# Kernel tuning notes

Measured on AMD Instinct MI355X. Metric: run time of the kernel, lower is better.

The kernel has to match this reference:

```python
import jax, jax.numpy as jnp
import numpy as np

N_NODES = 50000
N_EDGES = 800000
HIDDEN = 128
IN_DIM = 128
OUT_DIM = 1
N_LAYERS = 4
N_GRAPHS = 32
LN_EPS = 1e-5


def setup_inputs() -> dict:
    key = jax.random.key(0)
    ks = jax.random.split(key, 12)
    s = 1.0 / np.sqrt(HIDDEN)
    inp = {
        "x": jax.random.normal(ks[0], (N_NODES, IN_DIM), dtype=jnp.float32),
        "edge_index": jax.random.randint(ks[1], (2, N_EDGES), 0, N_NODES, dtype=jnp.int64),
        "batch": jnp.sort(jax.random.randint(ks[2], (N_NODES,), 0, N_GRAPHS, dtype=jnp.int64)),
        "W_emb": jax.random.normal(ks[3], (HIDDEN, IN_DIM), dtype=jnp.float32) * s,
        "b_emb": jax.random.normal(ks[4], (HIDDEN,), dtype=jnp.float32) * s,
        "W_layers": jax.random.normal(ks[5], (N_LAYERS, HIDDEN, HIDDEN), dtype=jnp.float32) * s,
        "b_layers": jax.random.normal(ks[6], (N_LAYERS, HIDDEN), dtype=jnp.float32) * s,
        "ln_gamma": 1.0 + 0.02 * jax.random.normal(ks[7], (N_LAYERS, HIDDEN), dtype=jnp.float32),
        "ln_beta": 0.02 * jax.random.normal(ks[8], (N_LAYERS, HIDDEN), dtype=jnp.float32),
        "W_out": jax.random.normal(ks[9], (OUT_DIM, HIDDEN), dtype=jnp.float32) * s,
    }
    return inp


def _layer_norm(x, gamma, beta):
    mu = jnp.mean(x, axis=-1, keepdims=True)
    var = jnp.mean(jnp.square(x - mu), axis=-1, keepdims=True)
    return (x - mu) * jax.lax.rsqrt(var + LN_EPS) * gamma + beta


def reference(x, edge_index, batch, W_emb, b_emb, W_layers, b_layers, ln_gamma, ln_beta, W_out):
    n = x.shape[0]
    # add self-loops (PyG GCNConv default)
    loop = jnp.arange(n, dtype=edge_index.dtype)
    row = jnp.concatenate([edge_index[0], loop])  # source nodes
    col = jnp.concatenate([edge_index[1], loop])  # target nodes
    # symmetric normalization: deg over targets
    deg = jax.ops.segment_sum(jnp.ones_like(col, dtype=x.dtype), col, num_segments=n)
    dis = jnp.where(deg > 0, jax.lax.rsqrt(jnp.maximum(deg, 1.0)), 0.0)
    norm = dis[row] * dis[col]  # [E+N]

    h = x @ W_emb.T + b_emb  # embedding layer
    for i in range(N_LAYERS):
        t = h @ W_layers[i].T                      # [N, H] linear first
        msg = t[row] * norm[:, None]               # gather + scale  [E+N, H]
        agg = jax.ops.segment_sum(msg, col, num_segments=n) + b_layers[i]
        h = _layer_norm(h + jax.nn.relu(agg), ln_gamma[i], ln_beta[i])

    out = h @ W_out.T                              # [N, OUT_DIM]
    sums = jax.ops.segment_sum(out, batch, num_segments=N_GRAPHS)
    cnts = jax.ops.segment_sum(jnp.ones((n,), out.dtype), batch, num_segments=N_GRAPHS)
    return sums / jnp.maximum(cnts, 1.0)[:, None]  # [N_GRAPHS, OUT_DIM]
```

## Files before the change

### kernel.cpp

```cpp
#include <hip/hip_runtime.h>
#include <hip/hip_fp16.h>

#define NN 50000
#define NE 800000
#define NETOT (NE + NN)
#define NH 128
#define NG 32
#define NL 4
#define NB 196
#define EMBB 782
#define HISTB 3125
#define PREP4B 256
#define LBLK 782
#define NTILE 12500
#define WSLOT (NH * NH)

typedef __attribute__((ext_vector_type(8))) short bf16x8;
typedef __attribute__((ext_vector_type(4))) float f32x4;
typedef __attribute__((ext_vector_type(2))) float f32x2;

__device__ inline short f2bf(float x) {
  union { float f; unsigned u; } v;
  v.f = x;
  unsigned r = v.u + 0x7FFF + ((v.u >> 16) & 1);
  return (short)(r >> 16);
}
__device__ inline float bf2f(short s) {
  union { unsigned u; float f; } v;
  v.u = ((unsigned)(unsigned short)s) << 16;
  return v.f;
}

__device__ inline int pdw(int t, int quad) {
  return (((2 * t + (quad >> 1)) & 3) << 3) + ((t >> 1) << 1) + (quad & 1);
}

__device__ inline void fp8row_fma(float (&ag)[4][8], uint4 qa, uint4 qb,
                                  float w) {
  const unsigned dw[8] = {qa.x, qa.y, qa.z, qa.w, qb.x, qb.y, qb.z, qb.w};
#pragma unroll
  for (int ks = 0; ks < 4; ++ks) {
    f32x2 u0 = __builtin_amdgcn_cvt_pk_f32_fp8(dw[2 * ks], 0);
    f32x2 u1 = __builtin_amdgcn_cvt_pk_f32_fp8(dw[2 * ks], 1);
    f32x2 u2 = __builtin_amdgcn_cvt_pk_f32_fp8(dw[2 * ks + 1], 0);
    f32x2 u3 = __builtin_amdgcn_cvt_pk_f32_fp8(dw[2 * ks + 1], 1);
    ag[ks][0] += u0.x * w; ag[ks][1] += u0.y * w;
    ag[ks][2] += u1.x * w; ag[ks][3] += u1.y * w;
    ag[ks][4] += u2.x * w; ag[ks][5] += u2.y * w;
    ag[ks][6] += u3.x * w; ag[ks][7] += u3.y * w;
  }
}

__device__ inline int block_exscan(int v) {
  __shared__ int wsum[4];
  int tid = threadIdx.x, wave = tid >> 6, lane = tid & 63;
  int x = v;
#pragma unroll
  for (int off = 1; off < 64; off <<= 1) {
    int y = __shfl_up(x, off, 64);
    if (lane >= off) x += y;
  }
  if (lane == 63) wsum[wave] = x;
  __syncthreads();
  int wp = 0;
  if (wave > 0) wp += wsum[0];
  if (wave > 1) wp += wsum[1];
  if (wave > 2) wp += wsum[2];
  return wp + x - v;
}

__global__ __launch_bounds__(256) void prep_hist_emb_kernel(
    const float* __restrict__ Xf, const float* __restrict__ W_emb,
    const float* __restrict__ W_layers, short* __restrict__ hi,
    short* __restrict__ lo, const int* __restrict__ row,
    const int* __restrict__ col, int* __restrict__ cnt4, int* __restrict__ rank,
    const float* __restrict__ bias, __half* __restrict__ hnew,
    unsigned char* __restrict__ h8) {
  __shared__ short Wh[WSLOT];
  __shared__ short Wl[WSLOT];
  int tid = threadIdx.x;
  int blk = blockIdx.x;
  if (blk >= EMBB) {
    if (blk < EMBB + HISTB) {
      int e = (blk - EMBB) * 256 + tid;
      if (e < NE) {
        int s = row[e];
        int t = s / NTILE;
        rank[e] = atomicAdd(&cnt4[col[e] * 4 + t], 1);
      }
    } else {
      int i = (blk - EMBB - HISTB) * 256 + tid;
      if (i < 4 * WSLOT) {
        int slot = i >> 14, f = i & (WSLOT - 1);
        int j = f & 7, lane = (f >> 3) & 63, tt = (f >> 9) & 7, ks = f >> 12;
        int n = tt * 16 + (lane & 15);
        int k = ks * 32 + ((lane >> 4) & 3) * 8 + j;
        const float* W = W_layers + (size_t)slot * WSLOT;
        float x = W[n * NH + k];
        short hh = f2bf(x);
        hi[i] = hh;
        lo[i] = f2bf(x - bf2f(hh));
      }
    }
    return;
  }

#pragma unroll
  for (int i = tid * 8; i < WSLOT; i += 256 * 8) {
    int f = i;
    int lane8 = (f >> 3) & 63, tt = (f >> 9) & 7, ks = f >> 12;
    int n = tt * 16 + (lane8 & 15);
    int k0 = ks * 32 + ((lane8 >> 4) & 3) * 8;
    const float* wr = W_emb + n * NH + k0;
    float4 a0 = *(const float4*)wr;
    float4 a1 = *(const float4*)(wr + 4);
    float wv[8] = {a0.x, a0.y, a0.z, a0.w, a1.x, a1.y, a1.z, a1.w};
    bf16x8 vh, vl;
#pragma unroll
    for (int j = 0; j < 8; ++j) {
      short hh = f2bf(wv[j]);
      vh[j] = hh;
      vl[j] = f2bf(wv[j] - bf2f(hh));
    }
    *(bf16x8*)&Wh[i] = vh;
    *(bf16x8*)&Wl[i] = vl;
  }
  __syncthreads();

  int wave = tid >> 6, lane = tid & 63;
  int quad = lane >> 4, r16 = lane & 15;
  int m0 = blk * 64 + wave * 16;
  if (m0 >= NN) return;
  int mA = m0 + r16;

  f32x4 acc[8];
#pragma unroll
  for (int t = 0; t < 8; ++t) acc[t] = (f32x4){0.f, 0.f, 0.f, 0.f};

#pragma unroll
  for (int ks = 0; ks < 4; ++ks) {
    int klane = ks * 32 + quad * 8;
    const float* xr = Xf + (size_t)mA * NH + klane;
    float4 a0 = *(const float4*)xr;
    float4 a1 = *(const float4*)(xr + 4);
    float af[8] = {a0.x, a0.y, a0.z, a0.w, a1.x, a1.y, a1.z, a1.w};
    bf16x8 xhi, xlo;
#pragma unroll
    for (int j = 0; j < 8; ++j) {
      short h = f2bf(af[j]);
      xhi[j] = h;
      xlo[j] = f2bf(af[j] - bf2f(h));
    }
#pragma unroll
    for (int t = 0; t < 8; ++t) {
      int fidx = ((ks * 8 + t) * 64 + lane) << 3;
      bf16x8 whi = *(const bf16x8*)&Wh[fidx];
      bf16x8 wlo = *(const bf16x8*)&Wl[fidx];
      acc[t] = __builtin_amdgcn_mfma_f32_16x16x32_bf16(whi, xhi, acc[t], 0, 0, 0);
      acc[t] = __builtin_amdgcn_mfma_f32_16x16x32_bf16(whi, xlo, acc[t], 0, 0, 0);
      acc[t] = __builtin_amdgcn_mfma_f32_16x16x32_bf16(wlo, xhi, acc[t], 0, 0, 0);
    }
  }

  int m = m0 + r16;
  int cb = quad * 4;
#pragma unroll
  for (int t = 0; t < 8; ++t) {
    int ch = t * 16 + cb;
    float4 bb = *(const float4*)(bias + ch);
    float o0 = acc[t][0] + bb.x, o1 = acc[t][1] + bb.y;
    float o2 = acc[t][2] + bb.z, o3 = acc[t][3] + bb.w;
    __half2 p01 = __float22half2_rn(make_float2(o0, o1));
    __half2 p23 = __float22half2_rn(make_float2(o2, o3));
    *(uint2*)(hnew + (size_t)m * NH + ch) =
        make_uint2(*(unsigned*)&p01, *(unsigned*)&p23);
    int v = 0;
    v = __builtin_amdgcn_cvt_pk_fp8_f32(o0, o1, v, 0);
    v = __builtin_amdgcn_cvt_pk_fp8_f32(o2, o3, v, 1);
    ((unsigned*)(h8 + (size_t)m * NH))[pdw(t, quad)] = (unsigned)v;
  }
}

__global__ __launch_bounds__(256) void scan1_kernel(const int* __restrict__ cnt4,
                                                    int* __restrict__ bsum,
                                                    float* __restrict__ dis,
                                                    int* __restrict__ deg) {
  int i = blockIdx.x * 256 + threadIdx.x;
  int v = 0;
  if (i < NN) {
    int4 c4 = *(const int4*)&cnt4[i * 4];
    v = c4.x + c4.y + c4.z + c4.w + 1;
    deg[i] = v;
    dis[i] = rsqrtf((float)v);
  }
  int lane = threadIdx.x & 63;
  int s = v;
#pragma unroll
  for (int off = 32; off; off >>= 1) s += __shfl_down(s, off, 64);
  __shared__ int ws[4];
  if (lane == 0) ws[threadIdx.x >> 6] = s;
  __syncthreads();
  if (threadIdx.x == 0) bsum[blockIdx.x] = ws[0] + ws[1] + ws[2] + ws[3];
}

__global__ __launch_bounds__(256) void scan3b_kernel(const int* __restrict__ deg,
                                                     const int* __restrict__ bsum,
                                                     const float* __restrict__ dis,
                                                     int* __restrict__ offs,
                                                     int2* __restrict__ csr) {
  __shared__ int ws2[4];
  int tid = threadIdx.x;
  int b = blockIdx.x;
  int v = (tid < NB && tid < b) ? bsum[tid] : 0;
  int lane = tid & 63;
  int s = v;
#pragma unroll
  for (int off = 32; off; off >>= 1) s += __shfl_down(s, off, 64);
  if (lane == 0) ws2[tid >> 6] = s;
  __syncthreads();
  int bo = ws2[0] + ws2[1] + ws2[2] + ws2[3];
  int i = b * 256 + tid;
  int c = (i < NN) ? deg[i] : 0;
  int ex = block_exscan(c);
  if (i < NN) {
    int o = bo + ex;
    offs[i] = o;
    float dii = dis[i];
    csr[o + c - 1] =
        make_int2((i << 6) | (i & 63), __float_as_int(dii * dii));
  }
}

__global__ __launch_bounds__(256) void fill_kernel(const int* __restrict__ row,
                                                   const int* __restrict__ col,
                                                   const int* __restrict__ rank,
                                                   const int* __restrict__ cnt4,
                                                   const float* __restrict__ dis,
                                                   const int* __restrict__ offs,
                                                   int2* __restrict__ csr) {
  int e = blockIdx.x * 256 + threadIdx.x;
  if (e < NE) {
    int d = col[e];
    int s = row[e];
    int t = s / NTILE;
    int4 c4 = *(const int4*)&cnt4[d * 4];
    int pre = (t > 0 ? c4.x : 0) + (t > 1 ? c4.y : 0) + (t > 2 ? c4.z : 0);
    int pos = offs[d] + pre + rank[e];
    csr[pos] =
        make_int2((s << 6) | (d & 63), __float_as_int(dis[s] * dis[d]));
  }
}

template <bool LAST>
__global__ __launch_bounds__(256) void layer_fused(
    const unsigned char* __restrict__ h8in, const short* __restrict__ Whi,
    const short* __restrict__ Wlo, const float* __restrict__ bias,
    const __half* __restrict__ hprev, const float* __restrict__ gamma,
    const float* __restrict__ beta, const float* __restrict__ Wout,
    const int* __restrict__ offs, const int2* __restrict__ csr,
    __half* __restrict__ hnew, unsigned char* __restrict__ h8out,
    float* __restrict__ nodeval) {
  int tid = threadIdx.x, wave = tid >> 6, lane = tid & 63;
  int quad = lane >> 4, r16 = lane & 15;
  int m0 = blockIdx.x * 64 + wave * 16;
  if (m0 >= NN) return;
  int nd = m0 + r16;

  float ag[4][8];
#pragma unroll
  for (int ks = 0; ks < 4; ++ks)
#pragma unroll
    for (int j = 0; j < 8; ++j) ag[ks][j] = 0.f;

  const char* rbase = (const char*)h8in + quad * 32;
  int s0 = offs[nd];
  int e1 = (nd + 1 < NN) ? offs[nd + 1] : NETOT;
  int j = s0;
  for (; j + 2 <= e1; j += 2) {
    int2 p0 = csr[j], p1 = csr[j + 1];
    const uint4* r0 = (const uint4*)(rbase + (size_t)(((unsigned)p0.x) >> 6) * NH);
    const uint4* r1 = (const uint4*)(rbase + (size_t)(((unsigned)p1.x) >> 6) * NH);
    uint4 a0 = r0[0], b0 = r0[1];
    uint4 a1 = r1[0], b1 = r1[1];
    fp8row_fma(ag, a0, b0, __int_as_float(p0.y));
    fp8row_fma(ag, a1, b1, __int_as_float(p1.y));
  }
  if (j < e1) {
    int2 p0 = csr[j];
    const uint4* r0 = (const uint4*)(rbase + (size_t)(((unsigned)p0.x) >> 6) * NH);
    uint4 a0 = r0[0], b0 = r0[1];
    fp8row_fma(ag, a0, b0, __int_as_float(p0.y));
  }

  f32x4 acc[8];
#pragma unroll
  for (int t = 0; t < 8; ++t) acc[t] = (f32x4){0.f, 0.f, 0.f, 0.f};

#pragma unroll
  for (int ks = 0; ks < 4; ++ks) {
    bf16x8 xhi, xlo;
#pragma unroll
    for (int q = 0; q < 8; ++q) {
      short hh = f2bf(ag[ks][q]);
      xhi[q] = hh;
      xlo[q] = f2bf(ag[ks][q] - bf2f(hh));
    }
#pragma unroll
    for (int t = 0; t < 8; ++t) {
      int fidx = ((ks * 8 + t) * 64 + lane) << 3;
      bf16x8 whi = *(const bf16x8*)&Whi[fidx];
      bf16x8 wlo = *(const bf16x8*)&Wlo[fidx];
      acc[t] = __builtin_amdgcn_mfma_f32_16x16x32_bf16(whi, xhi, acc[t], 0, 0, 0);
      acc[t] = __builtin_amdgcn_mfma_f32_16x16x32_bf16(whi, xlo, acc[t], 0, 0, 0);
      acc[t] = __builtin_amdgcn_mfma_f32_16x16x32_bf16(wlo, xhi, acc[t], 0, 0, 0);
    }
  }

  int m = nd;
  int cb = quad * 4;
  float vv[8][4];
  float s = 0.f, s2 = 0.f;
#pragma unroll
  for (int t = 0; t < 8; ++t) {
    int ch = t * 16 + cb;
    float4 bb = *(const float4*)(bias + ch);
    uint2 hp = *(const uint2*)(hprev + (size_t)m * NH + ch);
    float2 h01 = __half22float2(*(__half2*)&hp.x);
    float2 h23 = __half22float2(*(__half2*)&hp.y);
    float hv[4] = {h01.x, h01.y, h23.x, h23.y};
    float bb4[4] = {bb.x, bb.y, bb.z, bb.w};
#pragma unroll
    for (int r = 0; r < 4; ++r) {
      float z = fmaxf(acc[t][r] + bb4[r], 0.f);
      float val = hv[r] + z;
      vv[t][r] = val;
      s += val;
      s2 += val * val;
    }
  }
  s += __shfl_xor(s, 16, 64);
  s += __shfl_xor(s, 32, 64);
  s2 += __shfl_xor(s2, 16, 64);
  s2 += __shfl_xor(s2, 32, 64);
  float mean = s * (1.f / 128.f);
  float var = fmaxf(s2 * (1.f / 128.f) - mean * mean, 0.f);
  float inv = rsqrtf(var + 1e-5f);
  float d = 0.f;
#pragma unroll
  for (int t = 0; t < 8; ++t) {
    int ch = t * 16 + cb;
    float4 gv = *(const float4*)(gamma + ch);
    float4 bt = *(const float4*)(beta + ch);
    float o0 = (vv[t][0] - mean) * inv * gv.x + bt.x;
    float o1 = (vv[t][1] - mean) * inv * gv.y + bt.y;
    float o2 = (vv[t][2] - mean) * inv * gv.z + bt.z;
    float o3 = (vv[t][3] - mean) * inv * gv.w + bt.w;
    if (!LAST) {
      __half2 p01 = __float22half2_rn(make_float2(o0, o1));
      __half2 p23 = __float22half2_rn(make_float2(o2, o3));
      *(uint2*)(hnew + (size_t)m * NH + ch) =
          make_uint2(*(unsigned*)&p01, *(unsigned*)&p23);
      int pv = 0;
      pv = __builtin_amdgcn_cvt_pk_fp8_f32(o0, o1, pv, 0);
      pv = __builtin_amdgcn_cvt_pk_fp8_f32(o2, o3, pv, 1);
      ((unsigned*)(h8out + (size_t)m * NH))[pdw(t, quad)] = (unsigned)pv;
    } else {
      float4 wv = *(const float4*)(Wout + ch);
      d += o0 * wv.x + o1 * wv.y + o2 * wv.z + o3 * wv.w;
    }
  }
  if (LAST) {
    d += __shfl_xor(d, 16, 64);
    d += __shfl_xor(d, 32, 64);
    if (lane < 16) nodeval[m] = d;
  }
}

__global__ __launch_bounds__(256) void reduce_pool_kernel(
    const float* __restrict__ nodeval, const int* __restrict__ batch,
    float* __restrict__ gsum, int* __restrict__ gcnt, int* __restrict__ done,
    float* __restrict__ out) {
  __shared__ float bins[NG];
  __shared__ int cbins[NG];
  __shared__ int lastflag;
  int tid = threadIdx.x;
  if (tid < NG) {
    bins[tid] = 0.f;
    cbins[tid] = 0;
  }
  __syncthreads();
  int i = blockIdx.x * 256 + tid;
  if (i < NN) {
    int g = batch[i];
    atomicAdd(&bins[g], nodeval[i]);
    atomicAdd(&cbins[g], 1);
  }
  __syncthreads();
  if (tid < NG && cbins[tid]) {
    atomicAdd(&gsum[tid], bins[tid]);
    atomicAdd(&gcnt[tid], cbins[tid]);
  }
  __threadfence();
  if (tid == 0) lastflag = (atomicAdd(done, 1) == (int)gridDim.x - 1);
  __syncthreads();
  if (lastflag && tid < NG) {
    float sv = atomicAdd(&gsum[tid], 0.f);
    int cv = atomicAdd(&gcnt[tid], 0);
    out[tid] = sv / fmaxf((float)cv, 1.0f);
  }
}

extern "C" void kernel_launch(void* const* d_in, const int* in_sizes, int n_in,
                              void* d_out, int out_size, void* d_ws, size_t ws_size,
                              hipStream_t stream) {
  const float* x = (const float*)d_in[0];
  const int* eidx = (const int*)d_in[1];
  const int* batch = (const int*)d_in[2];
  const float* W_emb = (const float*)d_in[3];
  const float* b_emb = (const float*)d_in[4];
  const float* W_layers = (const float*)d_in[5];
  const float* b_layers = (const float*)d_in[6];
  const float* ln_gamma = (const float*)d_in[7];
  const float* ln_beta = (const float*)d_in[8];
  const float* W_out = (const float*)d_in[9];
  float* out = (float*)d_out;

  char* ws = (char*)d_ws;
  unsigned char* h8a = (unsigned char*)ws; ws += (size_t)NN * NH;
  unsigned char* h8b = (unsigned char*)ws; ws += (size_t)NN * NH;
  __half* h = (__half*)ws;      ws += (size_t)NN * NH * 2;
  short* Whi = (short*)ws;      ws += (size_t)4 * WSLOT * 2;
  short* Wlo = (short*)ws;      ws += (size_t)4 * WSLOT * 2;
  float* dis = (float*)ws;      ws += (size_t)NN * 4;
  int2* csr = (int2*)ws;        ws += (size_t)NETOT * 8;
  int* rank = (int*)ws;         ws += (size_t)NE * 4;
  int* offs = (int*)ws;         ws += (size_t)NN * 4;
  int* deg = (int*)ws;          ws += (size_t)NN * 4;
  float* nodeval = (float*)ws;  ws += (size_t)NN * 4;
  int* bsum = (int*)ws;         ws += (size_t)NB * 4;
  char* zero_base = ws;
  int* cnt4 = (int*)ws;         ws += (size_t)NN * 16;
  float* gsum = (float*)ws;     ws += (size_t)NG * 4;
  int* gcnt = (int*)ws;         ws += (size_t)NG * 4;
  int* done = (int*)ws;         ws += 64;
  size_t zero_bytes = (size_t)(ws - zero_base);
  hipMemsetAsync(zero_base, 0, zero_bytes, stream);

  const int* erow = eidx;
  const int* ecol = eidx + NE;

  prep_hist_emb_kernel<<<EMBB + HISTB + PREP4B, 256, 0, stream>>>(
      x, W_emb, W_layers, Whi, Wlo, erow, ecol, cnt4, rank, b_emb, h, h8a);
  scan1_kernel<<<NB, 256, 0, stream>>>(cnt4, bsum, dis, deg);
  scan3b_kernel<<<NB, 256, 0, stream>>>(deg, bsum, dis, offs, csr);
  fill_kernel<<<HISTB, 256, 0, stream>>>(erow, ecol, rank, cnt4, dis, offs, csr);

  for (int l = 0; l < NL; ++l) {
    const short* wh = Whi + (size_t)l * WSLOT;
    const short* wl = Wlo + (size_t)l * WSLOT;
    const float* bl = b_layers + (size_t)l * NH;
    const float* gl = ln_gamma + (size_t)l * NH;
    const float* be = ln_beta + (size_t)l * NH;
    const unsigned char* hin = (l & 1) ? h8b : h8a;
    unsigned char* hout = (l & 1) ? h8a : h8b;
    if (l == NL - 1)
      layer_fused<true><<<LBLK, 256, 0, stream>>>(
          hin, wh, wl, bl, h, gl, be, W_out, offs, csr, h, nullptr, nodeval);
    else
      layer_fused<false><<<LBLK, 256, 0, stream>>>(
          hin, wh, wl, bl, h, gl, be, nullptr, offs, csr, h, hout, nullptr);
  }
  reduce_pool_kernel<<<NB, 256, 0, stream>>>(nodeval, batch, gsum, gcnt, done,
                                             out);
}
```

Measured before the change: 363.7 us.

## Stage layer weights in LDS with 512-thread blocks and prefetch residual

```diff
diff --git a/kernel.cpp b/kernel.cpp
--- a/kernel.cpp
+++ b/kernel.cpp
@@ -11,7 +11,6 @@
 #define EMBB 782
 #define HISTB 3125
 #define PREP4B 256
-#define LBLK 782
 #define NTILE 12500
 #define WSLOT (NH * NH)
 
@@ -252,7 +251,7 @@
 }
 
 template <bool LAST>
-__global__ __launch_bounds__(256) void layer_fused(
+__global__ __launch_bounds__(512) void layer_fused(
     const unsigned char* __restrict__ h8in, const short* __restrict__ Whi,
     const short* __restrict__ Wlo, const float* __restrict__ bias,
     const __half* __restrict__ hprev, const float* __restrict__ gamma,
@@ -260,11 +259,26 @@
     const int* __restrict__ offs, const int2* __restrict__ csr,
     __half* __restrict__ hnew, unsigned char* __restrict__ h8out,
     float* __restrict__ nodeval) {
-  int tid = threadIdx.x, wave = tid >> 6, lane = tid & 63;
+  __shared__ short Wh[WSLOT];
+  __shared__ short Wl[WSLOT];
+  int tid = threadIdx.x;
+#pragma unroll
+  for (int i = tid * 8; i < WSLOT; i += 512 * 8) {
+    *(bf16x8*)&Wh[i] = *(const bf16x8*)(Whi + i);
+    *(bf16x8*)&Wl[i] = *(const bf16x8*)(Wlo + i);
+  }
+
+  int wave = tid >> 6, lane = tid & 63;
   int quad = lane >> 4, r16 = lane & 15;
-  int m0 = blockIdx.x * 64 + wave * 16;
-  if (m0 >= NN) return;
-  int nd = m0 + r16;
+  int m0 = blockIdx.x * 128 + wave * 16;
+  bool active = m0 < NN;
+  int nd = active ? m0 + r16 : 0;
+  int cb = quad * 4;
+
+  uint2 hp[8];
+#pragma unroll
+  for (int t = 0; t < 8; ++t)
+    hp[t] = *(const uint2*)(hprev + (size_t)nd * NH + t * 16 + cb);
 
   float ag[4][8];
 #pragma unroll
@@ -274,7 +288,7 @@
 
   const char* rbase = (const char*)h8in + quad * 32;
   int s0 = offs[nd];
-  int e1 = (nd + 1 < NN) ? offs[nd + 1] : NETOT;
+  int e1 = active ? ((nd + 1 < NN) ? offs[nd + 1] : NETOT) : s0;
   int j = s0;
   for (; j + 2 <= e1; j += 2) {
     int2 p0 = csr[j], p1 = csr[j + 1];
@@ -292,6 +306,10 @@
     fp8row_fma(ag, a0, b0, __int_as_float(p0.y));
   }
 
+  __syncthreads();
+
+  if (!active) return;
+
   f32x4 acc[8];
 #pragma unroll
   for (int t = 0; t < 8; ++t) acc[t] = (f32x4){0.f, 0.f, 0.f, 0.f};
@@ -308,8 +326,8 @@
 #pragma unroll
     for (int t = 0; t < 8; ++t) {
       int fidx = ((ks * 8 + t) * 64 + lane) << 3;
-      bf16x8 whi = *(const bf16x8*)&Whi[fidx];
-      bf16x8 wlo = *(const bf16x8*)&Wlo[fidx];
+      bf16x8 whi = *(const bf16x8*)&Wh[fidx];
+      bf16x8 wlo = *(const bf16x8*)&Wl[fidx];
       acc[t] = __builtin_amdgcn_mfma_f32_16x16x32_bf16(whi, xhi, acc[t], 0, 0, 0);
       acc[t] = __builtin_amdgcn_mfma_f32_16x16x32_bf16(whi, xlo, acc[t], 0, 0, 0);
       acc[t] = __builtin_amdgcn_mfma_f32_16x16x32_bf16(wlo, xhi, acc[t], 0, 0, 0);
@@ -317,16 +335,14 @@
   }
 
   int m = nd;
-  int cb = quad * 4;
   float vv[8][4];
   float s = 0.f, s2 = 0.f;
 #pragma unroll
   for (int t = 0; t < 8; ++t) {
     int ch = t * 16 + cb;
     float4 bb = *(const float4*)(bias + ch);
-    uint2 hp = *(const uint2*)(hprev + (size_t)m * NH + ch);
-    float2 h01 = __half22float2(*(__half2*)&hp.x);
-    float2 h23 = __half22float2(*(__half2*)&hp.y);
+    float2 h01 = __half22float2(*(__half2*)&hp[t].x);
+    float2 h23 = __half22float2(*(__half2*)&hp[t].y);
     float hv[4] = {h01.x, h01.y, h23.x, h23.y};
     float bb4[4] = {bb.x, bb.y, bb.z, bb.w};
 #pragma unroll
@@ -455,6 +471,7 @@
   scan3b_kernel<<<NB, 256, 0, stream>>>(deg, bsum, dis, offs, csr);
   fill_kernel<<<HISTB, 256, 0, stream>>>(erow, ecol, rank, cnt4, dis, offs, csr);
 
+  int gblk = (NN + 127) / 128;
   for (int l = 0; l < NL; ++l) {
     const short* wh = Whi + (size_t)l * WSLOT;
     const short* wl = Wlo + (size_t)l * WSLOT;
@@ -464,10 +481,10 @@
     const unsigned char* hin = (l & 1) ? h8b : h8a;
     unsigned char* hout = (l & 1) ? h8a : h8b;
     if (l == NL - 1)
-      layer_fused<true><<<LBLK, 256, 0, stream>>>(
+      layer_fused<true><<<gblk, 512, 0, stream>>>(
           hin, wh, wl, bl, h, gl, be, W_out, offs, csr, h, nullptr, nodeval);
     else
-      layer_fused<false><<<LBLK, 256, 0, stream>>>(
+      layer_fused<false><<<gblk, 512, 0, stream>>>(
           hin, wh, wl, bl, h, gl, be, nullptr, offs, csr, h, hout, nullptr);
   }
   reduce_pool_kernel<<<NB, 256, 0, stream>>>(nodeval, batch, gsum, gcnt, done,
```

Result: faster. 331.2 us (-9.0%).
